# Kernel tuning notes

Hardware: AMD Instinct MI355X
Metric: run time of the kernel (lower is better)

## Reference

```python
import jax, jax.numpy as jnp
import numpy as np

# Problem sizes (match input_specs)
B, D, N, M, C = 2, 128, 131072, 131072, 128
IGNORE = -1  # config.data.ignore_label


def setup_inputs() -> dict:
    key = jax.random.key(0)
    k1, k2, k3, k4, k5 = jax.random.split(key, 5)
    vb = jax.random.randint(k1, (N, 1), 0, B)
    vxyz = jax.random.randint(k2, (N, 3), 0, D)
    coords = jnp.concatenate([vb, vxyz], axis=1).astype(jnp.int32)  # (N,4) [b,x,y,z]
    qb = jax.random.randint(k3, (M, 1), 0, B).astype(jnp.float32)
    qxyz = jax.random.uniform(k4, (M, 3), minval=0.0, maxval=float(D - 1))
    query_points = jnp.concatenate([qb, qxyz], axis=1)  # (M,4) [b,x,y,z]
    features = jax.random.normal(k5, (N, C), dtype=jnp.float32)  # (N,C)
    return {"coords": coords, "features": features, "query_points": query_points}


def reference(coords, features, query_points):
    n_vox = coords.shape[0]
    b = coords[:, 0]
    xyz = coords[:, 1:]
    # per-batch coordinate shift (torch.amin per batch), scale_factor == 1
    shift = jax.ops.segment_min(xyz, b, num_segments=B)  # (B,3)
    xyz = xyz - shift[b]
    qb = query_points[:, 0].astype(jnp.int32)
    q = query_points[:, 1:] - shift[qb].astype(query_points.dtype)  # (M,3)

    # dense occupancy: voxel index at occupied cells, IGNORE elsewhere
    occ = jnp.full((B, D, D, D), IGNORE, dtype=jnp.int32)
    occ = occ.at[b, xyz[:, 0], xyz[:, 1], xyz[:, 2]].set(
        jnp.arange(n_vox, dtype=jnp.int32))

    # 8-corner trilinear gather
    q0 = jnp.floor(q)
    f = q - q0                              # fractional part, (M,3)
    q0i = q0.astype(jnp.int32)
    offs = jnp.array([[i, j, k] for i in (0, 1) for j in (0, 1) for k in (0, 1)],
                     dtype=jnp.int32)       # (8,3)
    corner = q0i[:, None, :] + offs[None]   # (M,8,3)
    inb = jnp.all((corner >= 0) & (corner < D), axis=-1)  # (M,8)
    cc = jnp.clip(corner, 0, D - 1)
    idx = occ[qb[:, None], cc[..., 0], cc[..., 1], cc[..., 2]]  # (M,8)

    # trilinear weights: prod over dims of f (corner==1) or 1-f (corner==0)
    w = jnp.prod(jnp.where(offs[None].astype(bool), f[:, None, :], 1.0 - f[:, None, :]),
                 axis=-1)                   # (M,8)
    valid = inb & (idx >= 0)
    wv = jnp.where(valid, w, 0.0)
    wsum = wv.sum(-1)                       # (M,)

    safe_idx = jnp.clip(idx, 0, None)
    gathered = features[safe_idx]           # (M,8,C)
    query_features = jnp.einsum('mk,mkc->mc', wv, gathered) / \
        jnp.maximum(wsum, 1e-8)[:, None]    # normalized by valid weight mass

    interpolation_indices = jnp.where(valid, idx, IGNORE)
    accum_voxel_weights = jax.ops.segment_sum(
        wv.reshape(-1), safe_idx.reshape(-1), num_segments=n_vox)
    return query_features, interpolation_indices, wv, accum_voxel_weights
```

## Files before the change

kernel.cpp:

```cpp
#include <hip/hip_runtime.h>
#include <limits.h>

#define NBATCH 2
#define DIM 128
#define NVOX 131072
#define NQ 131072
#define OCC_SIZE (NBATCH * DIM * DIM * DIM)

#define QF_OFF  0
#define IDX_OFF (NQ * 128)
#define WV_OFF  (IDX_OFF + NQ * 8)
#define ACC_OFF (WV_OFF + NQ * 8)

#define SHIFT_BLOCKS 64

#define WREDUCE_MIN(mv)                                       \
    _Pragma("unroll")                                         \
    for (int off = 32; off >= 1; off >>= 1)                   \
        mv = min(mv, __shfl_xor(mv, off, 64));

__global__ __launch_bounds__(256) void k_prep(const int* __restrict__ coords,
                                              int* __restrict__ sp,
                                              int* __restrict__ occ,
                                              float* __restrict__ accum) {
    int tid = blockIdx.x * 256 + threadIdx.x;
    int stride = gridDim.x * 256;
    for (int j = tid; j < NVOX; j += stride) accum[j] = 0.f;
    int4* occ4 = (int4*)occ;
    int4 neg1 = make_int4(-1, -1, -1, -1);
    for (int j = tid; j < OCC_SIZE / 4; j += stride) occ4[j] = neg1;

    if (blockIdx.x < SHIFT_BLOCKS) {
        __shared__ int sm[4][6];
        int i0 = blockIdx.x * 256 + threadIdx.x;
        int sstride = SHIFT_BLOCKS * 256;
        int m0 = INT_MAX, m1 = INT_MAX, m2 = INT_MAX;
        int m3 = INT_MAX, m4 = INT_MAX, m5 = INT_MAX;
        const int4* c4 = (const int4*)coords;
        for (int i = i0; i < NVOX; i += sstride) {
            int4 c = c4[i];
            if (c.x == 0) { m0 = min(m0, c.y); m1 = min(m1, c.z); m2 = min(m2, c.w); }
            else          { m3 = min(m3, c.y); m4 = min(m4, c.z); m5 = min(m5, c.w); }
        }
        WREDUCE_MIN(m0) WREDUCE_MIN(m1) WREDUCE_MIN(m2)
        WREDUCE_MIN(m3) WREDUCE_MIN(m4) WREDUCE_MIN(m5)
        int wave = threadIdx.x >> 6;
        if ((threadIdx.x & 63) == 0) {
            sm[wave][0] = m0; sm[wave][1] = m1; sm[wave][2] = m2;
            sm[wave][3] = m3; sm[wave][4] = m4; sm[wave][5] = m5;
        }
        __syncthreads();
        if (threadIdx.x == 0) {
            #pragma unroll
            for (int c = 0; c < 6; ++c) {
                int v = min(min(sm[0][c], sm[1][c]), min(sm[2][c], sm[3][c]));
                sp[c * SHIFT_BLOCKS + blockIdx.x] = v;
            }
        }
    }
}

__device__ __forceinline__ void load_shift(const int* __restrict__ sp, int* sh) {
    if (threadIdx.x < 64) {
        int l = threadIdx.x;
        #pragma unroll
        for (int c = 0; c < 6; ++c) {
            int v = sp[c * SHIFT_BLOCKS + l];
            WREDUCE_MIN(v)
            if (l == 0) sh[c] = v;
        }
    }
    __syncthreads();
}

__global__ __launch_bounds__(256) void k_build(const int* __restrict__ coords,
                                               const int* __restrict__ sp,
                                               int* __restrict__ occ) {
    __shared__ int sh[6];
    load_shift(sp, sh);
    int i = blockIdx.x * 256 + threadIdx.x;
    int4 c = ((const int4*)coords)[i];
    int b = c.x;
    int x = c.y - sh[b * 3 + 0];
    int y = c.z - sh[b * 3 + 1];
    int z = c.w - sh[b * 3 + 2];
    atomicMax(&occ[((b * DIM + x) * DIM + y) * DIM + z], i);
}

__global__ __launch_bounds__(256) void k_query(
    const float* __restrict__ qpts, const float* __restrict__ feats,
    const int* __restrict__ occ, const int* __restrict__ sp,
    float* __restrict__ out) {
    __shared__ int sh[6];
    load_shift(sp, sh);

    int lane = threadIdx.x & 63;
    int gwave = blockIdx.x * 4 + (threadIdx.x >> 6);
    int qbase = gwave * 8;

    int qi = lane >> 3, k = lane & 7;
    int q = qbase + qi;
    float4 qp = ((const float4*)qpts)[q];
    int qb = (int)qp.x;
    float qx = qp.y - (float)sh[qb * 3 + 0];
    float qy = qp.z - (float)sh[qb * 3 + 1];
    float qz = qp.w - (float)sh[qb * 3 + 2];
    float fx0 = floorf(qx), fy0 = floorf(qy), fz0 = floorf(qz);
    float fx = qx - fx0, fy = qy - fy0, fz = qz - fz0;
    int ox = (k >> 2) & 1, oy = (k >> 1) & 1, oz = k & 1;
    int cx = (int)fx0 + ox, cy = (int)fy0 + oy, cz = (int)fz0 + oz;
    bool inb = ((unsigned)cx < DIM) && ((unsigned)cy < DIM) && ((unsigned)cz < DIM);
    int ccx = min(max(cx, 0), DIM - 1);
    int ccy = min(max(cy, 0), DIM - 1);
    int ccz = min(max(cz, 0), DIM - 1);
    int idx = occ[((qb * DIM + ccx) * DIM + ccy) * DIM + ccz];
    float w = (ox ? fx : 1.f - fx) * (oy ? fy : 1.f - fy) * (oz ? fz : 1.f - fz);
    bool valid = inb && (idx >= 0);
    float wvk = valid ? w : 0.f;

    out[IDX_OFF + (size_t)qbase * 8 + lane] = valid ? (float)idx : -1.f;
    out[WV_OFF  + (size_t)qbase * 8 + lane] = wvk;
    if (valid && wvk != 0.f) atomicAdd(out + ACC_OFF + idx, wvk);

    float wsum = wvk;
    wsum += __shfl_xor(wsum, 1, 64);
    wsum += __shfl_xor(wsum, 2, 64);
    wsum += __shfl_xor(wsum, 4, 64);
    float inv = __builtin_amdgcn_rcpf(fmaxf(wsum, 1e-8f));

    int sidx = valid ? idx : 0;
    unsigned long long vm = __ballot(wvk != 0.f);
    const float2* f2 = (const float2*)feats;
    float2 acc[8];
#pragma unroll
    for (int g = 0; g < 8; ++g) { acc[g].x = 0.f; acc[g].y = 0.f; }
#pragma unroll
    for (int g = 0; g < 8; ++g) {
        unsigned int sub = (unsigned int)(vm >> (g * 8)) & 0xffu;
        while (sub) {
            int j = __ffs(sub) - 1; sub &= sub - 1;
            int src = g * 8 + j;
            float wv_j = __shfl(wvk, src, 64);
            int   idx_j = __shfl(sidx, src, 64);
            float2 fv = f2[(size_t)idx_j * 64 + lane];
            acc[g].x = fmaf(wv_j, fv.x, acc[g].x);
            acc[g].y = fmaf(wv_j, fv.y, acc[g].y);
        }
    }

    float2* qf = (float2*)(out + QF_OFF);
#pragma unroll
    for (int g = 0; g < 8; ++g) {
        float iv = __shfl(inv, g * 8, 64);
        float2 r;
        r.x = acc[g].x * iv;
        r.y = acc[g].y * iv;
        qf[(size_t)(qbase + g) * 64 + lane] = r;
    }
}

extern "C" void kernel_launch(void* const* d_in, const int* in_sizes, int n_in,
                              void* d_out, int out_size, void* d_ws, size_t ws_size,
                              hipStream_t stream) {
    const int*   coords = (const int*)d_in[0];
    const float* feats  = (const float*)d_in[1];
    const float* qpts   = (const float*)d_in[2];
    float* out = (float*)d_out;

    int* sp  = (int*)d_ws;
    int* occ = (int*)((char*)d_ws + 4096);

    k_prep<<<2048, 256, 0, stream>>>(coords, sp, occ, out + ACC_OFF);
    k_build<<<NVOX / 256, 256, 0, stream>>>(coords, sp, occ);
    k_query<<<NQ / 32, 256, 0, stream>>>(qpts, feats, occ, sp, out);
}
```

Before: 49.37 us.

## Replace dense occupancy grid with bitmap plus sparse index table

Replaces the 16 MB dense int occupancy grid, which had to be filled with -1 on every call, with a 512 KB occupancy bitmap and an index array that is only reset at the occupied cells. The build kernel now uses unshifted coordinates so it no longer waits on the shift reduction, and queries test the bitmap before loading the index. Output stores are switched to nontemporal. The idea relies on the shift being applied consistently to the query bounds checks, which makes the logic harder to follow and adds an extra atomicOr per voxel.

```diff
diff --git a/kernel.cpp b/kernel.cpp
--- a/kernel.cpp
+++ b/kernel.cpp
@@ -1,11 +1,11 @@
 #include <hip/hip_runtime.h>
 #include <limits.h>
 
-#define NBATCH 2
 #define DIM 128
 #define NVOX 131072
 #define NQ 131072
-#define OCC_SIZE (NBATCH * DIM * DIM * DIM)
+#define NCELL (2 * DIM * DIM * DIM)
+#define BITWORDS (NCELL / 64)
 
 #define QF_OFF  0
 #define IDX_OFF (NQ * 128)
@@ -14,21 +14,27 @@
 
 #define SHIFT_BLOCKS 64
 
+typedef float vf2 __attribute__((ext_vector_type(2)));
+
 #define WREDUCE_MIN(mv)                                       \
     _Pragma("unroll")                                         \
     for (int off = 32; off >= 1; off >>= 1)                   \
         mv = min(mv, __shfl_xor(mv, off, 64));
 
+__device__ __forceinline__ int cell_of(int b, int x, int y, int z) {
+    return (b << 21) + (x << 14) + (y << 7) + z;
+}
+
 __global__ __launch_bounds__(256) void k_prep(const int* __restrict__ coords,
                                               int* __restrict__ sp,
-                                              int* __restrict__ occ,
+                                              unsigned long long* __restrict__ bitmap,
+                                              int* __restrict__ idxg,
                                               float* __restrict__ accum) {
     int tid = blockIdx.x * 256 + threadIdx.x;
-    int stride = gridDim.x * 256;
-    for (int j = tid; j < NVOX; j += stride) accum[j] = 0.f;
-    int4* occ4 = (int4*)occ;
-    int4 neg1 = make_int4(-1, -1, -1, -1);
-    for (int j = tid; j < OCC_SIZE / 4; j += stride) occ4[j] = neg1;
+    int4 c = ((const int4*)coords)[tid];
+    idxg[cell_of(c.x, c.y, c.z, c.w)] = -1;
+    if (tid < BITWORDS) bitmap[tid] = 0ull;
+    accum[tid] = 0.f;
 
     if (blockIdx.x < SHIFT_BLOCKS) {
         __shared__ int sm[4][6];
@@ -38,9 +44,9 @@
         int m3 = INT_MAX, m4 = INT_MAX, m5 = INT_MAX;
         const int4* c4 = (const int4*)coords;
         for (int i = i0; i < NVOX; i += sstride) {
-            int4 c = c4[i];
-            if (c.x == 0) { m0 = min(m0, c.y); m1 = min(m1, c.z); m2 = min(m2, c.w); }
-            else          { m3 = min(m3, c.y); m4 = min(m4, c.z); m5 = min(m5, c.w); }
+            int4 v = c4[i];
+            if (v.x == 0) { m0 = min(m0, v.y); m1 = min(m1, v.z); m2 = min(m2, v.w); }
+            else          { m3 = min(m3, v.y); m4 = min(m4, v.z); m5 = min(m5, v.w); }
         }
         WREDUCE_MIN(m0) WREDUCE_MIN(m1) WREDUCE_MIN(m2)
         WREDUCE_MIN(m3) WREDUCE_MIN(m4) WREDUCE_MIN(m5)
@@ -52,45 +58,40 @@
         __syncthreads();
         if (threadIdx.x == 0) {
             #pragma unroll
-            for (int c = 0; c < 6; ++c) {
-                int v = min(min(sm[0][c], sm[1][c]), min(sm[2][c], sm[3][c]));
-                sp[c * SHIFT_BLOCKS + blockIdx.x] = v;
-            }
+            for (int k = 0; k < 6; ++k)
+                sp[k * SHIFT_BLOCKS + blockIdx.x] =
+                    min(min(sm[0][k], sm[1][k]), min(sm[2][k], sm[3][k]));
         }
     }
+}
+
+__global__ __launch_bounds__(256) void k_build(const int* __restrict__ coords,
+                                               unsigned long long* __restrict__ bitmap,
+                                               int* __restrict__ idxg) {
+    int i = blockIdx.x * 256 + threadIdx.x;
+    int4 c = ((const int4*)coords)[i];
+    int cell = cell_of(c.x, c.y, c.z, c.w);
+    atomicOr(&bitmap[cell >> 6], 1ull << (cell & 63));
+    atomicMax(&idxg[cell], i);
 }
 
 __device__ __forceinline__ void load_shift(const int* __restrict__ sp, int* sh) {
     if (threadIdx.x < 64) {
         int l = threadIdx.x;
         #pragma unroll
-        for (int c = 0; c < 6; ++c) {
-            int v = sp[c * SHIFT_BLOCKS + l];
+        for (int k = 0; k < 6; ++k) {
+            int v = sp[k * SHIFT_BLOCKS + l];
             WREDUCE_MIN(v)
-            if (l == 0) sh[c] = v;
+            if (l == 0) sh[k] = v;
         }
     }
     __syncthreads();
 }
 
-__global__ __launch_bounds__(256) void k_build(const int* __restrict__ coords,
-                                               const int* __restrict__ sp,
-                                               int* __restrict__ occ) {
-    __shared__ int sh[6];
-    load_shift(sp, sh);
-    int i = blockIdx.x * 256 + threadIdx.x;
-    int4 c = ((const int4*)coords)[i];
-    int b = c.x;
-    int x = c.y - sh[b * 3 + 0];
-    int y = c.z - sh[b * 3 + 1];
-    int z = c.w - sh[b * 3 + 2];
-    atomicMax(&occ[((b * DIM + x) * DIM + y) * DIM + z], i);
-}
-
 __global__ __launch_bounds__(256) void k_query(
     const float* __restrict__ qpts, const float* __restrict__ feats,
-    const int* __restrict__ occ, const int* __restrict__ sp,
-    float* __restrict__ out) {
+    const unsigned long long* __restrict__ bitmap, const int* __restrict__ idxg,
+    const int* __restrict__ sp, float* __restrict__ out) {
     __shared__ int sh[6];
     load_shift(sp, sh);
 
@@ -102,24 +103,30 @@
     int q = qbase + qi;
     float4 qp = ((const float4*)qpts)[q];
     int qb = (int)qp.x;
-    float qx = qp.y - (float)sh[qb * 3 + 0];
-    float qy = qp.z - (float)sh[qb * 3 + 1];
-    float qz = qp.w - (float)sh[qb * 3 + 2];
-    float fx0 = floorf(qx), fy0 = floorf(qy), fz0 = floorf(qz);
-    float fx = qx - fx0, fy = qy - fy0, fz = qz - fz0;
+    float fx0 = floorf(qp.y), fy0 = floorf(qp.z), fz0 = floorf(qp.w);
+    float fx = qp.y - fx0, fy = qp.z - fy0, fz = qp.w - fz0;
     int ox = (k >> 2) & 1, oy = (k >> 1) & 1, oz = k & 1;
-    int cx = (int)fx0 + ox, cy = (int)fy0 + oy, cz = (int)fz0 + oz;
-    bool inb = ((unsigned)cx < DIM) && ((unsigned)cy < DIM) && ((unsigned)cz < DIM);
-    int ccx = min(max(cx, 0), DIM - 1);
-    int ccy = min(max(cy, 0), DIM - 1);
-    int ccz = min(max(cz, 0), DIM - 1);
-    int idx = occ[((qb * DIM + ccx) * DIM + ccy) * DIM + ccz];
+    int ux = (int)fx0 + ox, uy = (int)fy0 + oy, uz = (int)fz0 + oz;
+    bool inb = ((unsigned)(ux - sh[qb * 3 + 0]) < DIM) &&
+               ((unsigned)(uy - sh[qb * 3 + 1]) < DIM) &&
+               ((unsigned)(uz - sh[qb * 3 + 2]) < DIM);
+    int cx = min(max(ux, 0), DIM - 1);
+    int cy = min(max(uy, 0), DIM - 1);
+    int cz = min(max(uz, 0), DIM - 1);
+    int cell = cell_of(qb, cx, cy, cz);
+    unsigned long long wbits = bitmap[cell >> 6];
+    bool occb = ((wbits >> (cell & 63)) & 1ull) != 0ull
+                && ((unsigned)ux < DIM) && ((unsigned)uy < DIM) && ((unsigned)uz < DIM);
+    bool valid = inb && occb;
+    int idx = 0;
+    if (valid) idx = idxg[cell];
+
     float w = (ox ? fx : 1.f - fx) * (oy ? fy : 1.f - fy) * (oz ? fz : 1.f - fz);
-    bool valid = inb && (idx >= 0);
     float wvk = valid ? w : 0.f;
 
-    out[IDX_OFF + (size_t)qbase * 8 + lane] = valid ? (float)idx : -1.f;
-    out[WV_OFF  + (size_t)qbase * 8 + lane] = wvk;
+    __builtin_nontemporal_store(valid ? (float)idx : -1.f,
+                                out + IDX_OFF + (size_t)qbase * 8 + lane);
+    __builtin_nontemporal_store(wvk, out + WV_OFF + (size_t)qbase * 8 + lane);
     if (valid && wvk != 0.f) atomicAdd(out + ACC_OFF + idx, wvk);
 
     float wsum = wvk;
@@ -130,10 +137,10 @@
 
     int sidx = valid ? idx : 0;
     unsigned long long vm = __ballot(wvk != 0.f);
-    const float2* f2 = (const float2*)feats;
-    float2 acc[8];
+    const vf2* f2 = (const vf2*)feats;
+    vf2 acc[8];
 #pragma unroll
-    for (int g = 0; g < 8; ++g) { acc[g].x = 0.f; acc[g].y = 0.f; }
+    for (int g = 0; g < 8; ++g) { acc[g] = (vf2){0.f, 0.f}; }
 #pragma unroll
     for (int g = 0; g < 8; ++g) {
         unsigned int sub = (unsigned int)(vm >> (g * 8)) & 0xffu;
@@ -142,20 +149,20 @@
             int src = g * 8 + j;
             float wv_j = __shfl(wvk, src, 64);
             int   idx_j = __shfl(sidx, src, 64);
-            float2 fv = f2[(size_t)idx_j * 64 + lane];
+            vf2 fv = f2[(size_t)idx_j * 64 + lane];
             acc[g].x = fmaf(wv_j, fv.x, acc[g].x);
             acc[g].y = fmaf(wv_j, fv.y, acc[g].y);
         }
     }
 
-    float2* qf = (float2*)(out + QF_OFF);
+    vf2* qf = (vf2*)(out + QF_OFF);
 #pragma unroll
     for (int g = 0; g < 8; ++g) {
         float iv = __shfl(inv, g * 8, 64);
-        float2 r;
+        vf2 r;
         r.x = acc[g].x * iv;
         r.y = acc[g].y * iv;
-        qf[(size_t)(qbase + g) * 64 + lane] = r;
+        __builtin_nontemporal_store(r, qf + (size_t)(qbase + g) * 64 + lane);
     }
 }
 
@@ -167,10 +174,11 @@
     const float* qpts   = (const float*)d_in[2];
     float* out = (float*)d_out;
 
-    int* sp  = (int*)d_ws;
-    int* occ = (int*)((char*)d_ws + 4096);
+    int* sp = (int*)d_ws;
+    unsigned long long* bitmap = (unsigned long long*)((char*)d_ws + 4096);
+    int* idxg = (int*)((char*)d_ws + 4096 + BITWORDS * 8);
 
-    k_prep<<<2048, 256, 0, stream>>>(coords, sp, occ, out + ACC_OFF);
-    k_build<<<NVOX / 256, 256, 0, stream>>>(coords, sp, occ);
-    k_query<<<NQ / 32, 256, 0, stream>>>(qpts, feats, occ, sp, out);
+    k_prep<<<NVOX / 256, 256, 0, stream>>>(coords, sp, bitmap, idxg, out + ACC_OFF);
+    k_build<<<NVOX / 256, 256, 0, stream>>>(coords, bitmap, idxg);
+    k_query<<<NQ / 32, 256, 0, stream>>>(qpts, feats, bitmap, idxg, sp, out);
 }
```

Measured after the change: 46.32 us. 1.07x faster.
